# Kernel optimization log

Hardware: AMD Instinct MI355X
Metric: run time of the kernel (lower is better)

The kernel has to match this reference:

```python
import jax, jax.numpy as jnp
import numpy as np

DIM = 1024
LN_EPS = 1e-5

def _layernorm(x, w, b):
    m = jnp.mean(x, axis=-1, keepdims=True)
    v = jnp.mean((x - m) ** 2, axis=-1, keepdims=True)
    return (x - m) * jax.lax.rsqrt(v + LN_EPS) * w + b

def _linear(x, w, b):
    # torch Linear: w is (out, in)
    return jnp.einsum('bsd,od->bso', x, w) + b

def setup_inputs() -> dict:
    key = jax.random.key(0)
    ks = jax.random.split(key, 8)
    d = DIM
    s = 0.02
    return {
        'x': jax.random.normal(ks[0], (4, 4096, d), dtype=jnp.float32),
        'ln1_w': jnp.ones((d,), jnp.float32), 'ln1_b': jnp.zeros((d,), jnp.float32),
        'ln2_w': jnp.ones((d,), jnp.float32), 'ln2_b': jnp.zeros((d,), jnp.float32),
        'gate_w': jax.random.normal(ks[1], (d, d), jnp.float32) * s,
        'gate_b': jnp.zeros((d,), jnp.float32),
        'val_w': jax.random.normal(ks[2], (d, d), jnp.float32) * s,
        'val_b': jnp.zeros((d,), jnp.float32),
        'ffn1_w': jax.random.normal(ks[3], (4 * d, d), jnp.float32) * s,
        'ffn1_b': jnp.zeros((4 * d,), jnp.float32),
        'ffn2_w': jax.random.normal(ks[4], (d, 4 * d), jnp.float32) * s,
        'ffn2_b': jnp.zeros((d,), jnp.float32),
    }

def reference(x, ln1_w, ln1_b, ln2_w, ln2_b, gate_w, gate_b, val_w, val_b, ffn1_w, ffn1_b, ffn2_w, ffn2_b):
    batch, seq_len, dim = x.shape
    h = _layernorm(x, ln1_w, ln1_b)
    g = jax.nn.sigmoid(_linear(h, gate_w, gate_b))
    v = _linear(h, val_w, val_b)
    cumsum_v = jnp.cumsum(g * v, axis=1)
    cumsum_g = jnp.cumsum(g, axis=1) + 1e-6
    position = jnp.arange(1, seq_len + 1, dtype=x.dtype)[None, :, None]  # [1,S,1]
    mem = cumsum_v / (jnp.sqrt(cumsum_g) * jnp.sqrt(position / seq_len + 0.1))
    x = x + mem
    h2 = _layernorm(x, ln2_w, ln2_b)
    ff = _linear(jax.nn.gelu(_linear(h2, ffn1_w, ffn1_b), approximate=False), ffn2_w, ffn2_b)
    return x + ff
```

## Files before the change

### kernel.cpp

```cpp
#include <hip/hip_runtime.h>
#include <cstdint>
#include <cstddef>

#define DIMD 1024
#define SEQ  4096
#define BATCH 4
#define MTOT (BATCH*SEQ)
#define NCHUNK 64
#define CLEN   64

typedef __attribute__((ext_vector_type(8))) short short8;
typedef __attribute__((ext_vector_type(4))) float floatx4;

__device__ __forceinline__ unsigned short f2bf(float f){
  unsigned u = __float_as_uint(f);
  u += 0x7fffu + ((u >> 16) & 1u);
  return (unsigned short)(u >> 16);
}
__device__ __forceinline__ float bf2f(unsigned short u){
  return __uint_as_float((unsigned)u << 16);
}

__device__ __forceinline__ float fast_sigmoid(float x){
  return __builtin_amdgcn_rcpf(1.f + __builtin_amdgcn_exp2f(-1.442695041f * x));
}
__device__ __forceinline__ float fast_gelu(float x){
  float u = 1.595769122f * x * (1.f + 0.044715f * x * x);
  return x * fast_sigmoid(u);
}

__device__ __forceinline__ void async16(const void* g, void* l){
  __builtin_amdgcn_global_load_lds(
      (const __attribute__((address_space(1))) void*)g,
      (__attribute__((address_space(3))) void*)l, 16, 0, 0);
}

__global__ void f32_to_bf16_kernel(const float* __restrict__ in,
                                   unsigned short* __restrict__ out, int n){
  int i = (blockIdx.x * 256 + threadIdx.x) * 4;
  if (i < n){
    float4 v = *(const float4*)(in + i);
    uint2 o;
    o.x = (unsigned)f2bf(v.x) | ((unsigned)f2bf(v.y) << 16);
    o.y = (unsigned)f2bf(v.z) | ((unsigned)f2bf(v.w) << 16);
    *(uint2*)(out + i) = o;
  }
}

__global__ __launch_bounds__(256)
void ln_kernel(const float* __restrict__ X, const float* __restrict__ w,
               const float* __restrict__ b, unsigned short* __restrict__ H){
  const int row = blockIdx.x;
  const int tid = threadIdx.x;
  const float4 xv = ((const float4*)(X + (size_t)row * DIMD))[tid];
  float s  = xv.x + xv.y + xv.z + xv.w;
  float ss = xv.x*xv.x + xv.y*xv.y + xv.z*xv.z + xv.w*xv.w;
  #pragma unroll
  for (int o = 32; o; o >>= 1){
    s  += __shfl_down(s, o);
    ss += __shfl_down(ss, o);
  }
  __shared__ float ps[4], pss[4], mv[2];
  const int wid = tid >> 6, lane = tid & 63;
  if (lane == 0){ ps[wid] = s; pss[wid] = ss; }
  __syncthreads();
  if (tid == 0){
    float S1 = ps[0]+ps[1]+ps[2]+ps[3];
    float S2 = pss[0]+pss[1]+pss[2]+pss[3];
    float m = S1 * (1.0f / DIMD);
    float var = S2 * (1.0f / DIMD) - m*m;
    mv[0] = m; mv[1] = rsqrtf(var + 1e-5f);
  }
  __syncthreads();
  const float m = mv[0], rs = mv[1];
  const float4 wv = ((const float4*)w)[tid];
  const float4 bv = ((const float4*)b)[tid];
  float o0 = (xv.x - m) * rs * wv.x + bv.x;
  float o1 = (xv.y - m) * rs * wv.y + bv.y;
  float o2 = (xv.z - m) * rs * wv.z + bv.z;
  float o3 = (xv.w - m) * rs * wv.w + bv.w;
  uint2 o;
  o.x = (unsigned)f2bf(o0) | ((unsigned)f2bf(o1) << 16);
  o.y = (unsigned)f2bf(o2) | ((unsigned)f2bf(o3) << 16);
  ((uint2*)(H + (size_t)row * DIMD))[tid] = o;
}

template<int EPI>
__global__ __launch_bounds__(512, 2)
void gemm256(const unsigned short* __restrict__ A, int lda,
             const unsigned short* __restrict__ Bw, int ldb,
             const float* __restrict__ bias, const float* __restrict__ bias2,
             void* __restrict__ OutP, void* __restrict__ Out2P,
             int ldc, int grid_n, int K)
{
  __shared__ char lds[3 * 32768];
  const int tid = threadIdx.x;
  const int bid = ((int)blockIdx.x & 7) * ((int)gridDim.x >> 3) + ((int)blockIdx.x >> 3);
  const int bm = bid / grid_n, bn = bid % grid_n;
  const int row0 = bm * 256, col0 = bn * 256;
  const int wid = tid >> 6, lane = tid & 63;
  const int wr = wid >> 2, wc = wid & 3;
  const int l15 = lane & 15, rq = lane >> 4;

  const int st_sl = (tid & 3) ^ ((tid >> 3) & 3);
  const unsigned short* aP = A  + (size_t)(row0 + (tid >> 2)) * lda + st_sl * 8;
  const unsigned short* bP = Bw + (size_t)(col0 + (tid >> 2)) * ldb + st_sl * 8;
  const int st_off = tid * 16;
  const size_t ldaL = (size_t)lda * 128, ldbL = (size_t)ldb * 128;

  const int slp = (rq ^ ((l15 >> 1) & 3)) << 4;
  int offA[8], offB[4];
  #pragma unroll
  for (int m = 0; m < 8; ++m) offA[m] = (wr*128 + m*16 + l15) * 64 + slp;
  #pragma unroll
  for (int n = 0; n < 4; ++n) offB[n] = 16384 + (wc*64 + n*16 + l15) * 64 + slp;

  floatx4 acc[8][4];
  #pragma unroll
  for (int m = 0; m < 8; ++m)
    #pragma unroll
    for (int n = 0; n < 4; ++n)
      acc[m][n] = (floatx4){0.f, 0.f, 0.f, 0.f};

  auto stage = [&](int buf, int kel){
    char* base = lds + buf * 32768;
    async16(aP + kel,        base + st_off);
    async16(aP + ldaL + kel, base + 8192  + st_off);
    async16(bP + kel,        base + 16384 + st_off);
    async16(bP + ldbL + kel, base + 24576 + st_off);
  };

  const int nt = K >> 5;
  stage(0, 0); stage(1, 32);
  asm volatile("s_waitcnt vmcnt(4)" ::: "memory");
  asm volatile("s_barrier" ::: "memory");

  int bufi = 0, sbuf = 2, kel = 64;
  for (int t = 0; t < nt; ++t){
    const char* Lp = lds + bufi * 32768;
    short8 av[8], bv[4];
    #pragma unroll
    for (int m = 0; m < 8; ++m) av[m] = *(const short8*)(Lp + offA[m]);
    #pragma unroll
    for (int n = 0; n < 4; ++n) bv[n] = *(const short8*)(Lp + offB[n]);

    stage(sbuf, kel);
    kel += 32;

    __builtin_amdgcn_s_setprio(1);
    #pragma unroll
    for (int m = 0; m < 8; ++m)
      #pragma unroll
      for (int n = 0; n < 4; ++n)
        acc[m][n] = __builtin_amdgcn_mfma_f32_16x16x32_bf16(av[m], bv[n], acc[m][n], 0, 0, 0);
    __builtin_amdgcn_s_setprio(0);

    asm volatile("s_barrier" ::: "memory");
    asm volatile("s_waitcnt vmcnt(4)" ::: "memory");
    asm volatile("s_barrier" ::: "memory");
    if (++bufi == 3) bufi = 0;
    if (++sbuf == 3) sbuf = 0;
  }

  asm volatile("s_waitcnt vmcnt(0)" ::: "memory");
  asm volatile("s_barrier" ::: "memory");

  if constexpr (EPI == 2 || EPI == 5){
    char* slab = lds + wid * 4096;
    unsigned short* dst; int colw; int ldout; bool sigm = false;
    const float* bsel;
    if constexpr (EPI == 5){
      const int c0 = col0 + wc * 64;
      if (c0 < 1024){ dst = (unsigned short*)OutP;  colw = c0;        bsel = bias;  sigm = true;  }
      else          { dst = (unsigned short*)Out2P; colw = c0 - 1024; bsel = bias2; sigm = false; }
      ldout = 1024;
    } else {
      dst = (unsigned short*)OutP; colw = col0 + wc * 64; bsel = bias; ldout = ldc;
    }
    const int rdrow = lane >> 3;
    const int rdoff  = rdrow * 128 + (((lane & 7) ^ (rdrow & 7)) << 4);
    const int rdoff2 = (rdrow + 8) * 128 + (((lane & 7) ^ ((rdrow + 8) & 7)) << 4);
    const int rdsl = (lane & 7) * 16;
    #pragma unroll
    for (int m = 0; m < 8; ++m){
      #pragma unroll
      for (int n = 0; n < 4; ++n){
        const float bs = bsel[colw + n*16 + l15];
        const int cchunk = n*2 + (l15 >> 3);
        #pragma unroll
        for (int j = 0; j < 4; ++j){
          const float val = acc[m][n][j] + bs;
          float r;
          if constexpr (EPI == 2){
            r = fast_gelu(val);
          } else {
            r = sigm ? fast_sigmoid(val) : val;
          }
          const int rr = rq*4 + j;
          *(unsigned short*)(slab + rr*128 + ((cchunk ^ (rr & 7)) << 4) + (l15 & 7)*2) = f2bf(r);
        }
      }
      asm volatile("s_waitcnt lgkmcnt(0)" ::: "memory");
      uint4 w0 = *(const uint4*)(slab + rdoff);
      uint4 w1 = *(const uint4*)(slab + rdoff2);
      asm volatile("s_waitcnt lgkmcnt(0)" ::: "memory");
      const int growb = row0 + wr * 128 + m * 16;
      *(uint4*)((char*)(dst + (size_t)(growb + rdrow) * ldout + colw) + rdsl) = w0;
      *(uint4*)((char*)(dst + (size_t)(growb + rdrow + 8) * ldout + colw) + rdsl) = w1;
    }
  } else {
    #pragma unroll
    for (int n = 0; n < 4; ++n){
      const int col = col0 + wc * 64 + n * 16 + l15;
      const float bs = (EPI == 4) ? 0.f : bias[col];
      #pragma unroll
      for (int m = 0; m < 8; ++m){
        const int rowb = row0 + wr * 128 + m * 16 + rq * 4;
        #pragma unroll
        for (int j = 0; j < 4; ++j){
          const size_t o = (size_t)(rowb + j) * ldc + col;
          float* O = (float*)OutP;
          O[o] = acc[m][n][j] + bs + O[o];
        }
      }
    }
  }
}

__global__ __launch_bounds__(256)
void scan_sums(const unsigned short* __restrict__ G, const unsigned short* __restrict__ V,
               float* __restrict__ SG, float* __restrict__ SGV){
  const int bc = blockIdx.x;
  const int d  = blockIdx.y * 256 + threadIdx.x;
  const int b = bc >> 6, c = bc & 63;
  size_t base = ((size_t)b * SEQ + (size_t)c * CLEN) * DIMD + d;
  float sg = 0.f, sgv = 0.f;
  for (int i = 0; i < CLEN; ++i){
    float g = bf2f(G[base + (size_t)i * DIMD]);
    float v = bf2f(V[base + (size_t)i * DIMD]);
    sg += g; sgv += g * v;
  }
  SG[(size_t)bc * DIMD + d] = sg;
  SGV[(size_t)bc * DIMD + d] = sgv;
}

__global__ __launch_bounds__(256)
void scan_prefix(float* __restrict__ SG, float* __restrict__ SGV){
  const int b = blockIdx.x;
  const int d = blockIdx.y * 256 + threadIdx.x;
  float rg = 0.f, rgv = 0.f;
  for (int c = 0; c < NCHUNK; ++c){
    size_t i = ((size_t)(b * NCHUNK + c)) * DIMD + d;
    float tg = SG[i], tv = SGV[i];
    SG[i] = rg; SGV[i] = rgv;
    rg += tg; rgv += tv;
  }
}

__global__ __launch_bounds__(256)
void scan_final(const unsigned short* __restrict__ G, const unsigned short* __restrict__ V,
                const float* __restrict__ SG, const float* __restrict__ SGV,
                const float* __restrict__ X, float* __restrict__ X2){
  const int bc = blockIdx.x;
  const int d  = blockIdx.y * 256 + threadIdx.x;
  const int b = bc >> 6, c = bc & 63;
  size_t base = ((size_t)b * SEQ + (size_t)c * CLEN) * DIMD + d;
  float rg  = SG[(size_t)bc * DIMD + d];
  float rgv = SGV[(size_t)bc * DIMD + d];
  for (int i = 0; i < CLEN; ++i){
    size_t idx = base + (size_t)i * DIMD;
    float g = bf2f(G[idx]), v = bf2f(V[idx]);
    rg += g; rgv += g * v;
    int s = c * CLEN + i;
    float pf = (float)(s + 1) * (1.0f / SEQ) + 0.1f;
    float mem = rgv * rsqrtf((rg + 1e-6f) * pf);
    X2[idx] = X[idx] + mem;
  }
}

extern "C" void kernel_launch(void* const* d_in, const int* in_sizes, int n_in,
                              void* d_out, int out_size, void* d_ws, size_t ws_size,
                              hipStream_t stream)
{
  const float* x     = (const float*)d_in[0];
  const float* ln1w  = (const float*)d_in[1];
  const float* ln1b  = (const float*)d_in[2];
  const float* ln2w  = (const float*)d_in[3];
  const float* ln2b  = (const float*)d_in[4];
  const float* gatew = (const float*)d_in[5];
  const float* gateb = (const float*)d_in[6];
  const float* valw  = (const float*)d_in[7];
  const float* valb  = (const float*)d_in[8];
  const float* f1w   = (const float*)d_in[9];
  const float* f1b   = (const float*)d_in[10];
  const float* f2w   = (const float*)d_in[11];
  const float* f2b   = (const float*)d_in[12];
  float* out = (float*)d_out;

  const size_t MB = 1024u * 1024u;
  const size_t baseNeed = (size_t)(32+32+32+2+2+8+8)*MB + 2u*BATCH*NCHUNK*DIMD*4 + 4096;
  const bool bigT = (baseNeed + 64u*MB) <= ws_size;

  char* ws = (char*)d_ws;
  size_t off = 0;
  auto alloc = [&](size_t bytes) -> char* {
    char* p = ws + off; off += (bytes + 255) & ~(size_t)255; return p;
  };
  unsigned short* H  = (unsigned short*)alloc((size_t)MTOT * DIMD * 2);
  unsigned short* G  = (unsigned short*)alloc((size_t)MTOT * DIMD * 2);
  unsigned short* V  = (unsigned short*)alloc((size_t)MTOT * DIMD * 2);
  if (bigT) alloc(64u * MB);
  unsigned short* T  = G;
  unsigned short* WGV= (unsigned short*)alloc((size_t)2 * DIMD * DIMD * 2);
  unsigned short* W1 = (unsigned short*)alloc((size_t)4 * DIMD * DIMD * 2);
  unsigned short* W2 = (unsigned short*)alloc((size_t)4 * DIMD * DIMD * 2);
  float* SG  = (float*)alloc((size_t)BATCH * NCHUNK * DIMD * 4);
  float* SGV = (float*)alloc((size_t)BATCH * NCHUNK * DIMD * 4);

  if (off > ws_size) return;

  f32_to_bf16_kernel<<<DIMD*DIMD/1024, 256, 0, stream>>>(gatew, WGV, DIMD*DIMD);
  f32_to_bf16_kernel<<<DIMD*DIMD/1024, 256, 0, stream>>>(valw,  WGV + (size_t)DIMD*DIMD, DIMD*DIMD);
  f32_to_bf16_kernel<<<4*DIMD*DIMD/1024, 256, 0, stream>>>(f1w, W1, 4*DIMD*DIMD);
  f32_to_bf16_kernel<<<4*DIMD*DIMD/1024, 256, 0, stream>>>(f2w, W2, 4*DIMD*DIMD);

  ln_kernel<<<MTOT, 256, 0, stream>>>(x, ln1w, ln1b, H);

  gemm256<5><<<(MTOT/256)*(2048/256), 512, 0, stream>>>(
      H, DIMD, WGV, DIMD, gateb, valb, G, V, 2048, 2048/256, DIMD);

  scan_sums  <<<dim3(BATCH*NCHUNK, DIMD/256), 256, 0, stream>>>(G, V, SG, SGV);
  scan_prefix<<<dim3(BATCH, DIMD/256),        256, 0, stream>>>(SG, SGV);
  scan_final <<<dim3(BATCH*NCHUNK, DIMD/256), 256, 0, stream>>>(G, V, SG, SGV, x, out);

  ln_kernel<<<MTOT, 256, 0, stream>>>(out, ln2w, ln2b, H);

  if (bigT){
    gemm256<2><<<(MTOT/256)*(4096/256), 512, 0, stream>>>(
        H, DIMD, W1, DIMD, f1b, nullptr, T, nullptr, 4*DIMD, 4096/256, DIMD);
    gemm256<3><<<(MTOT/256)*(DIMD/256), 512, 0, stream>>>(
        T, 4*DIMD, W2, 4*DIMD, f2b, nullptr, out, nullptr, DIMD, DIMD/256, 4*DIMD);
  } else {
    for (int c = 0; c < 2; ++c){
      const unsigned short* W1c = W1 + (size_t)c * 2048 * DIMD;
      const unsigned short* W2c = W2 + (size_t)c * 2048;
      gemm256<2><<<(MTOT/256)*(2048/256), 512, 0, stream>>>(
          H, DIMD, W1c, DIMD, f1b + c*2048, nullptr, T, nullptr, 2048, 2048/256, DIMD);
      if (c == 0)
        gemm256<3><<<(MTOT/256)*(DIMD/256), 512, 0, stream>>>(
            T, 2048, W2c, 4*DIMD, f2b, nullptr, out, nullptr, DIMD, DIMD/256, 2048);
      else
        gemm256<4><<<(MTOT/256)*(DIMD/256), 512, 0, stream>>>(
            T, 2048, W2c, 4*DIMD, nullptr, nullptr, out, nullptr, DIMD, DIMD/256, 2048);
    }
  }
}
```

Baseline: 504.0 us.

## Deepen GEMM LDS pipeline to four stages and interleave fragment loads with MFMA

The GEMM main loop moves from a 3-buffer to a 4-buffer LDS ring, so three K-tiles are in flight, and drops to a single wait and barrier per iteration. The 8x4 MFMA block is split into quadrants. The LDS fragment reads for the next quadrant, and for the next tile's first quadrant, are issued between MFMA groups to hide LDS latency behind matrix math. This raises LDS use to 128KB per block and register pressure from the double-buffered fragments. The last iterations issue redundant clamped loads.

```diff
diff --git a/kernel.cpp b/kernel.cpp
--- a/kernel.cpp
+++ b/kernel.cpp
@@ -93,7 +93,7 @@
              void* __restrict__ OutP, void* __restrict__ Out2P,
              int ldc, int grid_n, int K)
 {
-  __shared__ char lds[3 * 32768];
+  __shared__ char lds[4 * 32768];
   const int tid = threadIdx.x;
   const int bid = ((int)blockIdx.x & 7) * ((int)gridDim.x >> 3) + ((int)blockIdx.x >> 3);
   const int bm = bid / grid_n, bn = bid % grid_n;
@@ -131,35 +131,78 @@
   };
 
   const int nt = K >> 5;
-  stage(0, 0); stage(1, 32);
-  asm volatile("s_waitcnt vmcnt(4)" ::: "memory");
+  stage(0, 0); stage(1, 32); stage(2, 64);
+  asm volatile("s_waitcnt vmcnt(8)" ::: "memory");
   asm volatile("s_barrier" ::: "memory");
 
-  int bufi = 0, sbuf = 2, kel = 64;
+  short8 aLo[4], aHi[4], bLo[2], bHi[2];
+  {
+    const char* L0 = lds;
+    #pragma unroll
+    for (int m = 0; m < 4; ++m) aLo[m] = *(const short8*)(L0 + offA[m]);
+    bLo[0] = *(const short8*)(L0 + offB[0]);
+    bLo[1] = *(const short8*)(L0 + offB[1]);
+  }
+
   for (int t = 0; t < nt; ++t){
-    const char* Lp = lds + bufi * 32768;
-    short8 av[8], bv[4];
-    #pragma unroll
-    for (int m = 0; m < 8; ++m) av[m] = *(const short8*)(Lp + offA[m]);
-    #pragma unroll
-    for (int n = 0; n < 4; ++n) bv[n] = *(const short8*)(Lp + offB[n]);
-
-    stage(sbuf, kel);
-    kel += 32;
-
+    const char* L = lds + (t & 3) * 32768;
+
+    bHi[0] = *(const short8*)(L + offB[2]);
+    bHi[1] = *(const short8*)(L + offB[3]);
     __builtin_amdgcn_s_setprio(1);
     #pragma unroll
-    for (int m = 0; m < 8; ++m)
-      #pragma unroll
-      for (int n = 0; n < 4; ++n)
-        acc[m][n] = __builtin_amdgcn_mfma_f32_16x16x32_bf16(av[m], bv[n], acc[m][n], 0, 0, 0);
+    for (int mi = 0; mi < 4; ++mi)
+      #pragma unroll
+      for (int ni = 0; ni < 2; ++ni)
+        acc[mi][ni] = __builtin_amdgcn_mfma_f32_16x16x32_bf16(aLo[mi], bLo[ni], acc[mi][ni], 0, 0, 0);
     __builtin_amdgcn_s_setprio(0);
 
-    asm volatile("s_barrier" ::: "memory");
+    #pragma unroll
+    for (int mi = 0; mi < 4; ++mi) aHi[mi] = *(const short8*)(L + offA[4+mi]);
+    __builtin_amdgcn_s_setprio(1);
+    #pragma unroll
+    for (int mi = 0; mi < 4; ++mi)
+      #pragma unroll
+      for (int ni = 0; ni < 2; ++ni)
+        acc[mi][2+ni] = __builtin_amdgcn_mfma_f32_16x16x32_bf16(aLo[mi], bHi[ni], acc[mi][2+ni], 0, 0, 0);
+    __builtin_amdgcn_s_setprio(0);
+
+    __builtin_amdgcn_s_setprio(1);
+    #pragma unroll
+    for (int mi = 0; mi < 4; ++mi)
+      #pragma unroll
+      for (int ni = 0; ni < 2; ++ni)
+        acc[4+mi][2+ni] = __builtin_amdgcn_mfma_f32_16x16x32_bf16(aHi[mi], bHi[ni], acc[4+mi][2+ni], 0, 0, 0);
+    __builtin_amdgcn_s_setprio(0);
+
     asm volatile("s_waitcnt vmcnt(4)" ::: "memory");
     asm volatile("s_barrier" ::: "memory");
-    if (++bufi == 3) bufi = 0;
-    if (++sbuf == 3) sbuf = 0;
+    { const int kt = (t + 3 < nt) ? t + 3 : nt - 1;
+      stage((t + 3) & 3, kt << 5); }
+
+    if (t + 1 < nt){
+      const char* Ln = lds + ((t + 1) & 3) * 32768;
+      short8 b0 = *(const short8*)(Ln + offB[0]);
+      short8 b1 = *(const short8*)(Ln + offB[1]);
+      #pragma unroll
+      for (int mi = 0; mi < 4; ++mi) aLo[mi] = *(const short8*)(Ln + offA[mi]);
+      __builtin_amdgcn_s_setprio(1);
+      #pragma unroll
+      for (int mi = 0; mi < 4; ++mi)
+        #pragma unroll
+        for (int ni = 0; ni < 2; ++ni)
+          acc[4+mi][ni] = __builtin_amdgcn_mfma_f32_16x16x32_bf16(aHi[mi], bLo[ni], acc[4+mi][ni], 0, 0, 0);
+      __builtin_amdgcn_s_setprio(0);
+      bLo[0] = b0; bLo[1] = b1;
+    } else {
+      __builtin_amdgcn_s_setprio(1);
+      #pragma unroll
+      for (int mi = 0; mi < 4; ++mi)
+        #pragma unroll
+        for (int ni = 0; ni < 2; ++ni)
+          acc[4+mi][ni] = __builtin_amdgcn_mfma_f32_16x16x32_bf16(aHi[mi], bLo[ni], acc[4+mi][ni], 0, 0, 0);
+      __builtin_amdgcn_s_setprio(0);
+    }
   }
 
   asm volatile("s_waitcnt vmcnt(0)" ::: "memory");
```

Measured after the change: 514.7 us. 1.02x slower.

## Split GEMM main loop into four interleaved load/stage/MFMA quadrant phases

Applied to the files above, without the earlier changes.

Restructures the bf16 MFMA GEMM inner loop into four phases that each read part of the A/B fragments from LDS, issue one of the four async global-to-LDS copies for the tile two steps ahead, and run the matching quarter of the MFMAs. The goal is to spread memory traffic across the compute work and cut register pressure from holding all fragments at once. It adds several extra barriers per iteration, and it clamps the prefetch index at the tail, so the last iterations reload the final tile instead of reading past the end.

```diff
diff --git a/kernel.cpp b/kernel.cpp
--- a/kernel.cpp
+++ b/kernel.cpp
@@ -122,42 +122,85 @@
     for (int n = 0; n < 4; ++n)
       acc[m][n] = (floatx4){0.f, 0.f, 0.f, 0.f};
 
-  auto stage = [&](int buf, int kel){
+  auto stage1 = [&](int buf, int kel, int unit){
     char* base = lds + buf * 32768;
-    async16(aP + kel,        base + st_off);
-    async16(aP + ldaL + kel, base + 8192  + st_off);
-    async16(bP + kel,        base + 16384 + st_off);
-    async16(bP + ldbL + kel, base + 24576 + st_off);
+    if      (unit == 0) async16(aP + kel,        base + st_off);
+    else if (unit == 1) async16(aP + ldaL + kel, base + 8192  + st_off);
+    else if (unit == 2) async16(bP + kel,        base + 16384 + st_off);
+    else                async16(bP + ldbL + kel, base + 24576 + st_off);
   };
+  auto stage4 = [&](int buf, int kel){
+    #pragma unroll
+    for (int u = 0; u < 4; ++u) stage1(buf, kel, u);
+  };
 
   const int nt = K >> 5;
-  stage(0, 0); stage(1, 32);
+  stage4(0, 0); stage4(1, 32);
   asm volatile("s_waitcnt vmcnt(4)" ::: "memory");
   asm volatile("s_barrier" ::: "memory");
 
-  int bufi = 0, sbuf = 2, kel = 64;
+  int bufi = 0, sbuf = 2;
   for (int t = 0; t < nt; ++t){
     const char* Lp = lds + bufi * 32768;
-    short8 av[8], bv[4];
-    #pragma unroll
-    for (int m = 0; m < 8; ++m) av[m] = *(const short8*)(Lp + offA[m]);
-    #pragma unroll
-    for (int n = 0; n < 4; ++n) bv[n] = *(const short8*)(Lp + offB[n]);
-
-    stage(sbuf, kel);
-    kel += 32;
-
+    const int kel2 = ((t + 2 < nt) ? t + 2 : nt - 1) << 5;
+    short8 aLo[4], aHi[4], bLo[2], bHi[2];
+
+    #pragma unroll
+    for (int m = 0; m < 4; ++m) aLo[m] = *(const short8*)(Lp + offA[m]);
+    bLo[0] = *(const short8*)(Lp + offB[0]);
+    bLo[1] = *(const short8*)(Lp + offB[1]);
+    stage1(sbuf, kel2, 0);
+    asm volatile("s_barrier" ::: "memory");
+    asm volatile("s_waitcnt lgkmcnt(0)" ::: "memory");
     __builtin_amdgcn_s_setprio(1);
     #pragma unroll
-    for (int m = 0; m < 8; ++m)
-      #pragma unroll
-      for (int n = 0; n < 4; ++n)
-        acc[m][n] = __builtin_amdgcn_mfma_f32_16x16x32_bf16(av[m], bv[n], acc[m][n], 0, 0, 0);
+    for (int m = 0; m < 4; ++m)
+      #pragma unroll
+      for (int n = 0; n < 2; ++n)
+        acc[m][n] = __builtin_amdgcn_mfma_f32_16x16x32_bf16(aLo[m], bLo[n], acc[m][n], 0, 0, 0);
     __builtin_amdgcn_s_setprio(0);
-
-    asm volatile("s_barrier" ::: "memory");
+    asm volatile("s_barrier" ::: "memory");
+
+    bHi[0] = *(const short8*)(Lp + offB[2]);
+    bHi[1] = *(const short8*)(Lp + offB[3]);
+    stage1(sbuf, kel2, 1);
+    asm volatile("s_barrier" ::: "memory");
+    asm volatile("s_waitcnt lgkmcnt(0)" ::: "memory");
+    __builtin_amdgcn_s_setprio(1);
+    #pragma unroll
+    for (int m = 0; m < 4; ++m)
+      #pragma unroll
+      for (int n = 0; n < 2; ++n)
+        acc[m][2+n] = __builtin_amdgcn_mfma_f32_16x16x32_bf16(aLo[m], bHi[n], acc[m][2+n], 0, 0, 0);
+    __builtin_amdgcn_s_setprio(0);
+    asm volatile("s_barrier" ::: "memory");
+
+    #pragma unroll
+    for (int m = 0; m < 4; ++m) aHi[m] = *(const short8*)(Lp + offA[4+m]);
+    stage1(sbuf, kel2, 2);
+    asm volatile("s_barrier" ::: "memory");
+    asm volatile("s_waitcnt lgkmcnt(0)" ::: "memory");
+    __builtin_amdgcn_s_setprio(1);
+    #pragma unroll
+    for (int m = 0; m < 4; ++m)
+      #pragma unroll
+      for (int n = 0; n < 2; ++n)
+        acc[4+m][2+n] = __builtin_amdgcn_mfma_f32_16x16x32_bf16(aHi[m], bHi[n], acc[4+m][2+n], 0, 0, 0);
+    __builtin_amdgcn_s_setprio(0);
+    asm volatile("s_barrier" ::: "memory");
+
+    stage1(sbuf, kel2, 3);
+    asm volatile("s_barrier" ::: "memory");
+    __builtin_amdgcn_s_setprio(1);
+    #pragma unroll
+    for (int m = 0; m < 4; ++m)
+      #pragma unroll
+      for (int n = 0; n < 2; ++n)
+        acc[4+m][n] = __builtin_amdgcn_mfma_f32_16x16x32_bf16(aHi[m], bLo[n], acc[4+m][n], 0, 0, 0);
+    __builtin_amdgcn_s_setprio(0);
     asm volatile("s_waitcnt vmcnt(4)" ::: "memory");
     asm volatile("s_barrier" ::: "memory");
+
     if (++bufi == 3) bufi = 0;
     if (++sbuf == 3) sbuf = 0;
   }
```

New measurement: 500.7 us (median of 2 runs). About the same (-0.7%).
